# Kernel optimization log

Measured on AMD Instinct MI355X. Metric: run time of the kernel, lower is better.

Reference implementation:

```python
import jax, jax.numpy as jnp
import numpy as np

B, S, D = 4, 1024, 1024
H = 16
HD = D // H  # 64
NPOS = 64


def setup_inputs() -> dict:
    key = jax.random.key(0)
    ks = jax.random.split(key, 12)
    f = lambda k, shape, s=0.02: jax.random.normal(k, shape, dtype=jnp.float32) * s
    return {
        "q": jax.random.normal(ks[0], (B, S, D), dtype=jnp.float32),
        "k": jax.random.normal(ks[1], (B, S, D), dtype=jnp.float32),
        "v": jax.random.normal(ks[2], (B, S, D), dtype=jnp.float32),
        "Wq_w": f(ks[3], (D, D)), "Wq_b": f(ks[4], (D,)),
        "Wk_w": f(ks[5], (D, D)), "Wk_b": f(ks[6], (D,)),
        "Wv_w": f(ks[7], (D, D)), "Wv_b": f(ks[8], (D,)),
        "Wo_w": f(ks[9], (D, D)), "Wo_b": f(ks[10], (D,)),
        "pos_emb": f(ks[11], (HD, NPOS)),  # torch param is [1,1,head_dim,npos_max]
    }


def _proj(x, w, b):
    # nn.Linear: x @ w.T + b, then split heads -> [B, H, S, HD]
    y = jnp.einsum("bsd,ed->bse", x, w) + b
    bsz, s, _ = y.shape
    return y.reshape(bsz, s, H, HD).transpose(0, 2, 1, 3)


def reference(q, k, v, Wq_w, Wq_b, Wk_w, Wk_b, Wv_w, Wv_b, Wo_w, Wo_b, pos_emb):
    Q = _proj(q, Wq_w, Wq_b)
    K = _proj(k, Wk_w, Wk_b)
    V = _proj(v, Wv_w, Wv_b)

    scale = 1.0 / np.sqrt(HD).astype(np.float32)
    logits = jnp.einsum("bhqd,bhkd->bhqk", Q, K) * scale  # [B,H,S,S]

    # CoPE: sigmoid gates -> reverse cumsum -> interpolated position-logit gather
    gates = jax.nn.sigmoid(logits)
    pos = jnp.flip(jnp.cumsum(jnp.flip(gates, axis=-1), axis=-1), axis=-1)
    pos = jnp.minimum(pos, NPOS - 1)
    pos_floor = jnp.floor(pos)
    pos_ceil = jnp.ceil(pos)
    logits_int = jnp.einsum("bhqd,dn->bhqn", Q, pos_emb)  # [B,H,S,NPOS]
    lc = jnp.take_along_axis(logits_int, pos_ceil.astype(jnp.int32), axis=-1)
    lf = jnp.take_along_axis(logits_int, pos_floor.astype(jnp.int32), axis=-1)
    w = pos - pos_floor
    logits = logits + lc * w + lf * (1.0 - w)

    score = jax.nn.softmax(logits, axis=-1)
    out = jnp.einsum("bhqk,bhkd->bhqd", score, V)
    out = out.transpose(0, 2, 1, 3).reshape(q.shape[0], q.shape[1], D)
    return jnp.einsum("bsd,ed->bse", out, Wo_w) + Wo_b
```

## Files before the change

### kernel.cpp

```cpp
#include <hip/hip_runtime.h>
#include <hip/hip_bf16.h>

typedef __attribute__((ext_vector_type(8))) short short8;
typedef __attribute__((ext_vector_type(4))) float f32x4;
typedef unsigned short us;

#define MFMA16(a,b,c) __builtin_amdgcn_mfma_f32_16x16x32_bf16((a),(b),(c),0,0,0)
#define LOG2E 1.4426950408889634f

static __device__ __forceinline__ us bf16r(float x){
  unsigned u = __builtin_bit_cast(unsigned, x);
  u = u + 0x7fffu + ((u >> 16) & 1u);
  return (us)(u >> 16);
}
static __device__ __forceinline__ unsigned cvtpk(float a, float b){
  unsigned r; asm("v_cvt_pk_bf16_f32 %0, %1, %2" : "=v"(r) : "v"(a), "v"(b)); return r;
}
static __device__ __forceinline__ short8 cvt8(float4 a, float4 b){
  uint4 u; u.x = cvtpk(a.x, a.y); u.y = cvtpk(a.z, a.w);
  u.z = cvtpk(b.x, b.y); u.w = cvtpk(b.z, b.w);
  return __builtin_bit_cast(short8, u);
}
static __device__ __forceinline__ float b2f(us h){
  return __builtin_bit_cast(float, (unsigned)h << 16);
}
static __device__ __forceinline__ float exp2fast(float x){
  float r; asm("v_exp_f32 %0, %1" : "=v"(r) : "v"(x)); return r;
}
static __device__ __forceinline__ float rcpfast(float x){
  float r; asm("v_rcp_f32 %0, %1" : "=v"(r) : "v"(x)); return r;
}
static __device__ __forceinline__ float fractfast(float x){
  float r; asm("v_fract_f32 %0, %1" : "=v"(r) : "v"(x)); return r;
}

__global__ __launch_bounds__(256)
void transpose_pe(const float* __restrict__ pe, us* __restrict__ peT){
  const int t = threadIdx.x;
  const int n = t & 63, dq = t >> 6;
#pragma unroll
  for (int j = 0; j < 16; ++j){
    const int d = dq * 16 + j;
    peT[n * 64 + d] = bf16r(pe[d * 64 + n] * LOG2E);
  }
}

__global__ __launch_bounds__(256)
void transpose_v(const us* __restrict__ Vb, us* __restrict__ VT){
  __shared__ __align__(16) us tile[64 * 72];
  const int t = threadIdx.x;
  const int stile = blockIdx.x & 15;
  const int bh = blockIdx.x >> 4;
  const int b = bh >> 4, h = bh & 15;
  const int s0 = stile << 6;
#pragma unroll
  for (int c = 0; c < 2; ++c){
    const int idx = t + (c << 8);
    const int sr = idx >> 3, cw = idx & 7;
    *(short8*)&tile[sr * 72 + cw * 8] =
        *(const short8*)(Vb + ((size_t)(b * 1024 + s0 + sr)) * 1024 + h * 64 + cw * 8);
  }
  __syncthreads();
#pragma unroll
  for (int c = 0; c < 2; ++c){
    const int idx = t + (c << 8);
    const int dr = idx >> 3, sw = idx & 7;
    short8 o;
#pragma unroll
    for (int j = 0; j < 8; ++j) o[j] = (short)tile[(sw * 8 + j) * 72 + dr];
    *(short8*)(VT + ((size_t)(bh * 64 + dr)) * 1024 + s0 + sw * 8) = o;
  }
}

template<bool A_BF16, bool OUT_BF16>
__global__ __launch_bounds__(256)
void gemm3(const void* __restrict__ Av0, const void* __restrict__ Av1, const void* __restrict__ Av2,
           const float* __restrict__ W0, const float* __restrict__ W1, const float* __restrict__ W2,
           const float* __restrict__ bp0, const float* __restrict__ bp1, const float* __restrict__ bp2,
           void* __restrict__ O0, void* __restrict__ O1, void* __restrict__ O2){
  __shared__ __align__(16) us Al[128 * 64];
  __shared__ __align__(16) us Bl[128 * 64];
  const int sel = blockIdx.y;
  const void* Av   = sel == 0 ? Av0 : (sel == 1 ? Av1 : Av2);
  const float* Wm  = sel == 0 ? W0  : (sel == 1 ? W1  : W2);
  const float* bias = sel == 0 ? bp0 : (sel == 1 ? bp1 : bp2);
  void* Ov         = sel == 0 ? O0  : (sel == 1 ? O1  : O2);
  const int tid = threadIdx.x;
  const int bm = blockIdx.x & 31, bn = blockIdx.x >> 5;
  const int m0 = bm << 7, n0 = bn << 7;
  const int w = tid >> 6, l = tid & 63;
  const int lr = l & 15, lg = l >> 4;
  const int wm = (w & 1) << 6, wn = (w >> 1) << 6;
  int srow[4], scol[4], sdst[4];
#pragma unroll
  for (int c = 0; c < 4; ++c){
    const int idx = tid + (c << 8);
    const int r = idx >> 3, cw = idx & 7;
    srow[c] = r; scol[c] = cw << 3;
    sdst[c] = r * 64 + ((cw << 3) ^ ((r & 7) << 3));
  }
  const int swz = (lr & 7) << 3;
  f32x4 acc[4][4];
#pragma unroll
  for (int i = 0; i < 4; ++i)
#pragma unroll
    for (int j = 0; j < 4; ++j) acc[i][j] = (f32x4){0.f, 0.f, 0.f, 0.f};

  auto ldA = [&](int c, int k) -> short8 {
    if constexpr (A_BF16){
      return *(const short8*)((const us*)Av + (size_t)(m0 + srow[c]) * 1024 + k + scol[c]);
    } else {
      const float* p = (const float*)Av + (size_t)(m0 + srow[c]) * 1024 + k + scol[c];
      return cvt8(*(const float4*)p, *(const float4*)(p + 4));
    }
  };
  auto ldW = [&](int c, int k) -> short8 {
    const float* p = Wm + (size_t)(n0 + srow[c]) * 1024 + k + scol[c];
    return cvt8(*(const float4*)p, *(const float4*)(p + 4));
  };

  short8 av[4], bv[4];
#pragma unroll
  for (int c = 0; c < 4; ++c){ av[c] = ldA(c, 0); bv[c] = ldW(c, 0); }

  for (int k0 = 0; k0 < 1024; k0 += 64){
    __syncthreads();
#pragma unroll
    for (int c = 0; c < 4; ++c){
      *(short8*)&Al[sdst[c]] = av[c];
      *(short8*)&Bl[sdst[c]] = bv[c];
    }
    __syncthreads();
    if (k0 < 960){
#pragma unroll
      for (int c = 0; c < 4; ++c){ av[c] = ldA(c, k0 + 64); bv[c] = ldW(c, k0 + 64); }
    }
#pragma unroll
    for (int ks = 0; ks < 2; ++ks){
      short8 af[4], bfv[4];
#pragma unroll
      for (int mt = 0; mt < 4; ++mt)
        af[mt] = *(const short8*)&Al[(wm + mt * 16 + lr) * 64 + (((ks << 5) + (lg << 3)) ^ swz)];
#pragma unroll
      for (int nt = 0; nt < 4; ++nt)
        bfv[nt] = *(const short8*)&Bl[(wn + nt * 16 + lr) * 64 + (((ks << 5) + (lg << 3)) ^ swz)];
#pragma unroll
      for (int mt = 0; mt < 4; ++mt)
#pragma unroll
        for (int nt = 0; nt < 4; ++nt)
          acc[mt][nt] = MFMA16(af[mt], bfv[nt], acc[mt][nt]);
    }
  }
  float bb[4];
#pragma unroll
  for (int nt = 0; nt < 4; ++nt) bb[nt] = bias[n0 + wn + nt * 16 + lr];
#pragma unroll
  for (int mt = 0; mt < 4; ++mt)
#pragma unroll
    for (int nt = 0; nt < 4; ++nt)
#pragma unroll
      for (int r = 0; r < 4; ++r){
        const size_t m = m0 + wm + mt * 16 + lg * 4 + r;
        const size_t n = n0 + wn + nt * 16 + lr;
        const float vv = acc[mt][nt][r] + bb[nt];
        if (OUT_BF16) ((us*)Ov)[m * 1024 + n] = bf16r(vv);
        else          ((float*)Ov)[m * 1024 + n] = vv;
      }
}

__global__ __launch_bounds__(256, 5)
void cope_attn_v6(const us* __restrict__ Qb, const us* __restrict__ Kb,
                  const us* __restrict__ VT, const us* __restrict__ peT,
                  us* __restrict__ Ob){
  __shared__ __align__(16) us yl[16 * 1024];
  const int tid = threadIdx.x;
  const int w = tid >> 6, l = tid & 63;
  const int lr = l & 15, lg = l >> 4;
  const int qt = blockIdx.x & 63;
  const int bh = blockIdx.x >> 6;
  const int b = bh >> 4, h = bh & 15;
  const int q0 = qt << 4;
  const us* Qh = Qb + ((size_t)(b * 1024 + q0)) * 1024 + h * 64;
  const us* Kh = Kb + ((size_t)(b * 1024)) * 1024 + h * 64;
  const us* Vh = VT + ((size_t)bh) * 64 * 1024;
  const float QSC = 0.125f * LOG2E;

  const short8 aq0 = *(const short8*)(Qh + (size_t)lr * 1024 + lg * 8);
  const short8 aq1 = *(const short8*)(Qh + (size_t)lr * 1024 + 32 + lg * 8);

  {
    f32x4 a = (f32x4){0.f, 0.f, 0.f, 0.f};
    const short8 p0 = *(const short8*)(peT + (size_t)(w * 16 + lr) * 64 + lg * 8);
    const short8 p1 = *(const short8*)(peT + (size_t)(w * 16 + lr) * 64 + 32 + lg * 8);
    a = MFMA16(aq0, p0, a);
    a = MFMA16(aq1, p1, a);
#pragma unroll
    for (int r = 0; r < 4; ++r) yl[(lg * 4 + r) * 64 + w * 16 + lr] = bf16r(a[r]);
  }
  __syncthreads();
  unsigned trow[4];
#pragma unroll
  for (int rr = 0; rr < 4; ++rr){
    const int row = w * 4 + rr;
    const us lov = yl[row * 64 + l];
    const us hiv = (l < 63) ? yl[row * 64 + l + 1] : lov;
    const float dif = b2f(hiv) - b2f(lov);
    trow[rr] = (unsigned)lov | ((unsigned)bf16r(dif) << 16);
  }
  __syncthreads();
  {
    const int kbase = w << 8;
    const us* Kw = Kh + (size_t)(kbase + lr) * 1024 + lg * 8;
    short8 b0 = *(const short8*)(Kw);
    short8 b1 = *(const short8*)(Kw + 32);
    for (int t = 0; t < 16; ++t){
      short8 n0v = b0, n1v = b1;
      if (t < 15){
        const us* Kn = Kw + (size_t)((t + 1) * 16) * 1024;
        n0v = *(const short8*)(Kn);
        n1v = *(const short8*)(Kn + 32);
      }
      f32x4 a = (f32x4){0.f, 0.f, 0.f, 0.f};
      a = MFMA16(aq0, b0, a);
      a = MFMA16(aq1, b1, a);
      const int kc = kbase + t * 16 + lr;
      const unsigned p01 = cvtpk(a[0] * QSC, a[1] * QSC);
      const unsigned p23 = cvtpk(a[2] * QSC, a[3] * QSC);
      const int r0 = lg * 4;
      yl[(r0 + 0) * 1024 + (((kc >> 3) ^ ((r0 + 0) & 7)) << 3) + (kc & 7)] = (us)p01;
      yl[(r0 + 1) * 1024 + (((kc >> 3) ^ ((r0 + 1) & 7)) << 3) + (kc & 7)] = (us)(p01 >> 16);
      yl[(r0 + 2) * 1024 + (((kc >> 3) ^ ((r0 + 2) & 7)) << 3) + (kc & 7)] = (us)p23;
      yl[(r0 + 3) * 1024 + (((kc >> 3) ^ ((r0 + 3) & 7)) << 3) + (kc & 7)] = (us)(p23 >> 16);
      b0 = n0v; b1 = n1v;
    }
  }
  __syncthreads();
#pragma unroll
  for (int rr = 0; rr < 4; ++rr){
    const int row = w * 4 + rr;
    const int sz = row & 7;
    const int ad0 = row * 1024 + (((2 * l) ^ sz) << 3);
    const int ad1 = row * 1024 + (((2 * l + 1) ^ sz) << 3);
    const short8 y0 = *(const short8*)&yl[ad0];
    const short8 y1 = *(const short8*)&yl[ad1];
    float x[16];
#pragma unroll
    for (int j = 0; j < 8; ++j){ x[j] = b2f((us)y0[j]); x[8 + j] = b2f((us)y1[j]); }
    float pref[16];
    float s = 0.f;
#pragma unroll
    for (int i = 0; i < 16; ++i){
      const float g = rcpfast(1.f + exp2fast(-x[i]));
      pref[i] = s;
      s += g;
    }
    float run = s;
#pragma unroll
    for (int off = 1; off < 64; off <<= 1){
      const float t2 = __shfl_up(run, off);
      if (l >= off) run += t2;
    }
    const float T = __shfl(run, 63);
    const float base = T - (run - s);
    const unsigned tbl = trow[rr];
    float sum = 0.f;
#pragma unroll
    for (int i = 0; i < 16; ++i){
      float p = base - pref[i];
      p = __builtin_amdgcn_fmed3f(p, 0.f, 63.f);
      const int il = (int)p;
      const float wt = fractfast(p);
      const unsigned pr = (unsigned)__builtin_amdgcn_ds_bpermute(il << 2, (int)tbl);
      const float lo  = __builtin_bit_cast(float, pr << 16);
      const float dif = __builtin_bit_cast(float, pr & 0xffff0000u);
      const float e = exp2fast(x[i] + lo + wt * dif);
      x[i] = e;
      sum += e;
    }
#pragma unroll
    for (int off = 1; off < 64; off <<= 1) sum += __shfl_xor(sum, off);
    const float inv = rcpfast(sum);
    uint4 ua, ub;
    ua.x = cvtpk(x[0] * inv,  x[1] * inv);  ua.y = cvtpk(x[2] * inv,  x[3] * inv);
    ua.z = cvtpk(x[4] * inv,  x[5] * inv);  ua.w = cvtpk(x[6] * inv,  x[7] * inv);
    ub.x = cvtpk(x[8] * inv,  x[9] * inv);  ub.y = cvtpk(x[10] * inv, x[11] * inv);
    ub.z = cvtpk(x[12] * inv, x[13] * inv); ub.w = cvtpk(x[14] * inv, x[15] * inv);
    *(uint4*)&yl[ad0] = ua;
    *(uint4*)&yl[ad1] = ub;
  }
  __syncthreads();
  {
    const int d0 = w * 16;
    const int psw = lr & 7;
    f32x4 a = (f32x4){0.f, 0.f, 0.f, 0.f};
    const us* Vw = Vh + (size_t)(d0 + lr) * 1024 + lg * 8;
    short8 vb = *(const short8*)(Vw);
    for (int ks = 0; ks < 32; ++ks){
      short8 vn = vb;
      if (ks < 31) vn = *(const short8*)(Vw + (ks + 1) * 32);
      const short8 pa = *(const short8*)&yl[lr * 1024 + ((((ks << 2) + lg) ^ psw) << 3)];
      a = MFMA16(pa, vb, a);
      vb = vn;
    }
#pragma unroll
    for (int r = 0; r < 4; ++r)
      Ob[((size_t)(b * 1024 + q0 + lg * 4 + r)) * 1024 + h * 64 + d0 + lr] = bf16r(a[r]);
  }
}

extern "C" void kernel_launch(void* const* d_in, const int* in_sizes, int n_in,
                              void* d_out, int out_size, void* d_ws, size_t ws_size,
                              hipStream_t stream) {
  const float* q    = (const float*)d_in[0];
  const float* k    = (const float*)d_in[1];
  const float* v    = (const float*)d_in[2];
  const float* Wq_w = (const float*)d_in[3];
  const float* Wq_b = (const float*)d_in[4];
  const float* Wk_w = (const float*)d_in[5];
  const float* Wk_b = (const float*)d_in[6];
  const float* Wv_w = (const float*)d_in[7];
  const float* Wv_b = (const float*)d_in[8];
  const float* Wo_w = (const float*)d_in[9];
  const float* Wo_b = (const float*)d_in[10];
  const float* pe   = (const float*)d_in[11];
  float* out = (float*)d_out;

  char* W = (char*)d_ws;
  const size_t MB = (size_t)1 << 20;
  us* Qbf = (us*)(W);
  us* Kbf = (us*)(W + 8 * MB);
  us* Vbf = (us*)(W + 16 * MB);
  us* VTb = (us*)(W + 24 * MB);
  us* Obf = (us*)(W + 32 * MB);
  us* peT = (us*)(W + 40 * MB);

  transpose_pe<<<1, 256, 0, stream>>>(pe, peT);
  gemm3<false, true><<<dim3(256, 3), 256, 0, stream>>>(
      q, k, v, Wq_w, Wk_w, Wv_w, Wq_b, Wk_b, Wv_b, Qbf, Kbf, Vbf);
  transpose_v<<<1024, 256, 0, stream>>>(Vbf, VTb);
  cope_attn_v6<<<4096, 256, 0, stream>>>(Qbf, Kbf, VTb, peT, Obf);
  gemm3<true, false><<<dim3(256, 1), 256, 0, stream>>>(
      Obf, Obf, Obf, Wo_w, Wo_w, Wo_w, Wo_b, Wo_b, Wo_b, out, out, out);
}
```

Baseline: 221.1 us.

## Split attention key range into two chunks to halve LDS and raise occupancy

The attention kernel now processes the 1024 keys in two 512-key chunks, last chunk first. A carry of the reverse cumulative gate sum links the chunks, and the unnormalized softmax numerators are accumulated into the PV output. Normalization is deferred to the end using per-row sums kept in shared memory. This halves the LDS score buffer (32KB to 16KB) and raises launch bounds from 5 to 7 blocks per CU to improve occupancy. The costs are extra barriers and an unnormalized exp without max subtraction, so overflow risk is unchanged but bf16 rounding now happens before normalization.

```diff
diff --git a/kernel.cpp b/kernel.cpp
--- a/kernel.cpp
+++ b/kernel.cpp
@@ -168,11 +168,12 @@
       }
 }
 
-__global__ __launch_bounds__(256, 5)
-void cope_attn_v6(const us* __restrict__ Qb, const us* __restrict__ Kb,
+__global__ __launch_bounds__(256, 7)
+void cope_attn_v7(const us* __restrict__ Qb, const us* __restrict__ Kb,
                   const us* __restrict__ VT, const us* __restrict__ peT,
                   us* __restrict__ Ob){
-  __shared__ __align__(16) us yl[16 * 1024];
+  __shared__ __align__(16) us yl[16 * 512];
+  __shared__ float sums[16];
   const int tid = threadIdx.x;
   const int w = tid >> 6, l = tid & 63;
   const int lr = l & 15, lg = l >> 4;
@@ -207,104 +208,113 @@
     const float dif = b2f(hiv) - b2f(lov);
     trow[rr] = (unsigned)lov | ((unsigned)bf16r(dif) << 16);
   }
+
+  float carry[4] = {0.f, 0.f, 0.f, 0.f};
+  float rsum[4]  = {0.f, 0.f, 0.f, 0.f};
+  f32x4 oacc = (f32x4){0.f, 0.f, 0.f, 0.f};
+  const int d0 = w * 16;
+  const int psw = lr & 7;
+
+  for (int c = 1; c >= 0; --c){
+    const int koff = c << 9;
+    __syncthreads();
+    {
+      const int kbase = w << 7;
+      const us* Kw = Kh + (size_t)(koff + kbase + lr) * 1024 + lg * 8;
+      short8 b0 = *(const short8*)(Kw);
+      short8 b1 = *(const short8*)(Kw + 32);
+      for (int t = 0; t < 8; ++t){
+        short8 n0v = b0, n1v = b1;
+        if (t < 7){
+          const us* Kn = Kw + (size_t)((t + 1) * 16) * 1024;
+          n0v = *(const short8*)(Kn);
+          n1v = *(const short8*)(Kn + 32);
+        }
+        f32x4 a = (f32x4){0.f, 0.f, 0.f, 0.f};
+        a = MFMA16(aq0, b0, a);
+        a = MFMA16(aq1, b1, a);
+        const int kc = kbase + t * 16 + lr;
+        const unsigned p01 = cvtpk(a[0] * QSC, a[1] * QSC);
+        const unsigned p23 = cvtpk(a[2] * QSC, a[3] * QSC);
+        const int r0 = lg * 4;
+        yl[(r0 + 0) * 512 + (((kc >> 3) ^ ((r0 + 0) & 7)) << 3) + (kc & 7)] = (us)p01;
+        yl[(r0 + 1) * 512 + (((kc >> 3) ^ ((r0 + 1) & 7)) << 3) + (kc & 7)] = (us)(p01 >> 16);
+        yl[(r0 + 2) * 512 + (((kc >> 3) ^ ((r0 + 2) & 7)) << 3) + (kc & 7)] = (us)p23;
+        yl[(r0 + 3) * 512 + (((kc >> 3) ^ ((r0 + 3) & 7)) << 3) + (kc & 7)] = (us)(p23 >> 16);
+        b0 = n0v; b1 = n1v;
+      }
+    }
+    __syncthreads();
+#pragma unroll
+    for (int rr = 0; rr < 4; ++rr){
+      const int row = w * 4 + rr;
+      const int ad = row * 512 + ((l ^ (row & 7)) << 3);
+      const short8 y0 = *(const short8*)&yl[ad];
+      float x[8];
+#pragma unroll
+      for (int j = 0; j < 8; ++j) x[j] = b2f((us)y0[j]);
+      float pref[8];
+      float s = 0.f;
+#pragma unroll
+      for (int i = 0; i < 8; ++i){
+        const float g = rcpfast(1.f + exp2fast(-x[i]));
+        pref[i] = s;
+        s += g;
+      }
+      float run = s;
+#pragma unroll
+      for (int off = 1; off < 64; off <<= 1){
+        const float t2 = __shfl_up(run, off);
+        if (l >= off) run += t2;
+      }
+      const float T = __shfl(run, 63);
+      const float base = carry[rr] + T - (run - s);
+      carry[rr] += T;
+      const unsigned tbl = trow[rr];
+      float sum = 0.f;
+#pragma unroll
+      for (int i = 0; i < 8; ++i){
+        float p = base - pref[i];
+        p = __builtin_amdgcn_fmed3f(p, 0.f, 63.f);
+        const int il = (int)p;
+        const float wt = fractfast(p);
+        const unsigned pr = (unsigned)__builtin_amdgcn_ds_bpermute(il << 2, (int)tbl);
+        const float lo  = __builtin_bit_cast(float, pr << 16);
+        const float dif = __builtin_bit_cast(float, pr & 0xffff0000u);
+        const float e = exp2fast(x[i] + lo + wt * dif);
+        x[i] = e;
+        sum += e;
+      }
+      rsum[rr] += sum;
+      uint4 ua;
+      ua.x = cvtpk(x[0], x[1]); ua.y = cvtpk(x[2], x[3]);
+      ua.z = cvtpk(x[4], x[5]); ua.w = cvtpk(x[6], x[7]);
+      *(uint4*)&yl[ad] = ua;
+      if (c == 0){
+        float rs = rsum[rr];
+#pragma unroll
+        for (int off = 1; off < 64; off <<= 1) rs += __shfl_xor(rs, off);
+        if (l == 0) sums[row] = rs;
+      }
+    }
+    __syncthreads();
+    {
+      const us* Vw = Vh + (size_t)(d0 + lr) * 1024 + koff + lg * 8;
+      short8 vb = *(const short8*)(Vw);
+      for (int ks = 0; ks < 16; ++ks){
+        short8 vn = vb;
+        if (ks < 15) vn = *(const short8*)(Vw + (ks + 1) * 32);
+        const short8 pa = *(const short8*)&yl[lr * 512 + ((((ks << 2) + lg) ^ psw) << 3)];
+        oacc = MFMA16(pa, vb, oacc);
+        vb = vn;
+      }
+    }
+  }
   __syncthreads();
-  {
-    const int kbase = w << 8;
-    const us* Kw = Kh + (size_t)(kbase + lr) * 1024 + lg * 8;
-    short8 b0 = *(const short8*)(Kw);
-    short8 b1 = *(const short8*)(Kw + 32);
-    for (int t = 0; t < 16; ++t){
-      short8 n0v = b0, n1v = b1;
-      if (t < 15){
-        const us* Kn = Kw + (size_t)((t + 1) * 16) * 1024;
-        n0v = *(const short8*)(Kn);
-        n1v = *(const short8*)(Kn + 32);
-      }
-      f32x4 a = (f32x4){0.f, 0.f, 0.f, 0.f};
-      a = MFMA16(aq0, b0, a);
-      a = MFMA16(aq1, b1, a);
-      const int kc = kbase + t * 16 + lr;
-      const unsigned p01 = cvtpk(a[0] * QSC, a[1] * QSC);
-      const unsigned p23 = cvtpk(a[2] * QSC, a[3] * QSC);
-      const int r0 = lg * 4;
-      yl[(r0 + 0) * 1024 + (((kc >> 3) ^ ((r0 + 0) & 7)) << 3) + (kc & 7)] = (us)p01;
-      yl[(r0 + 1) * 1024 + (((kc >> 3) ^ ((r0 + 1) & 7)) << 3) + (kc & 7)] = (us)(p01 >> 16);
-      yl[(r0 + 2) * 1024 + (((kc >> 3) ^ ((r0 + 2) & 7)) << 3) + (kc & 7)] = (us)p23;
-      yl[(r0 + 3) * 1024 + (((kc >> 3) ^ ((r0 + 3) & 7)) << 3) + (kc & 7)] = (us)(p23 >> 16);
-      b0 = n0v; b1 = n1v;
-    }
-  }
-  __syncthreads();
-#pragma unroll
-  for (int rr = 0; rr < 4; ++rr){
-    const int row = w * 4 + rr;
-    const int sz = row & 7;
-    const int ad0 = row * 1024 + (((2 * l) ^ sz) << 3);
-    const int ad1 = row * 1024 + (((2 * l + 1) ^ sz) << 3);
-    const short8 y0 = *(const short8*)&yl[ad0];
-    const short8 y1 = *(const short8*)&yl[ad1];
-    float x[16];
-#pragma unroll
-    for (int j = 0; j < 8; ++j){ x[j] = b2f((us)y0[j]); x[8 + j] = b2f((us)y1[j]); }
-    float pref[16];
-    float s = 0.f;
-#pragma unroll
-    for (int i = 0; i < 16; ++i){
-      const float g = rcpfast(1.f + exp2fast(-x[i]));
-      pref[i] = s;
-      s += g;
-    }
-    float run = s;
-#pragma unroll
-    for (int off = 1; off < 64; off <<= 1){
-      const float t2 = __shfl_up(run, off);
-      if (l >= off) run += t2;
-    }
-    const float T = __shfl(run, 63);
-    const float base = T - (run - s);
-    const unsigned tbl = trow[rr];
-    float sum = 0.f;
-#pragma unroll
-    for (int i = 0; i < 16; ++i){
-      float p = base - pref[i];
-      p = __builtin_amdgcn_fmed3f(p, 0.f, 63.f);
-      const int il = (int)p;
-      const float wt = fractfast(p);
-      const unsigned pr = (unsigned)__builtin_amdgcn_ds_bpermute(il << 2, (int)tbl);
-      const float lo  = __builtin_bit_cast(float, pr << 16);
-      const float dif = __builtin_bit_cast(float, pr & 0xffff0000u);
-      const float e = exp2fast(x[i] + lo + wt * dif);
-      x[i] = e;
-      sum += e;
-    }
-#pragma unroll
-    for (int off = 1; off < 64; off <<= 1) sum += __shfl_xor(sum, off);
-    const float inv = rcpfast(sum);
-    uint4 ua, ub;
-    ua.x = cvtpk(x[0] * inv,  x[1] * inv);  ua.y = cvtpk(x[2] * inv,  x[3] * inv);
-    ua.z = cvtpk(x[4] * inv,  x[5] * inv);  ua.w = cvtpk(x[6] * inv,  x[7] * inv);
-    ub.x = cvtpk(x[8] * inv,  x[9] * inv);  ub.y = cvtpk(x[10] * inv, x[11] * inv);
-    ub.z = cvtpk(x[12] * inv, x[13] * inv); ub.w = cvtpk(x[14] * inv, x[15] * inv);
-    *(uint4*)&yl[ad0] = ua;
-    *(uint4*)&yl[ad1] = ub;
-  }
-  __syncthreads();
-  {
-    const int d0 = w * 16;
-    const int psw = lr & 7;
-    f32x4 a = (f32x4){0.f, 0.f, 0.f, 0.f};
-    const us* Vw = Vh + (size_t)(d0 + lr) * 1024 + lg * 8;
-    short8 vb = *(const short8*)(Vw);
-    for (int ks = 0; ks < 32; ++ks){
-      short8 vn = vb;
-      if (ks < 31) vn = *(const short8*)(Vw + (ks + 1) * 32);
-      const short8 pa = *(const short8*)&yl[lr * 1024 + ((((ks << 2) + lg) ^ psw) << 3)];
-      a = MFMA16(pa, vb, a);
-      vb = vn;
-    }
-#pragma unroll
-    for (int r = 0; r < 4; ++r)
-      Ob[((size_t)(b * 1024 + q0 + lg * 4 + r)) * 1024 + h * 64 + d0 + lr] = bf16r(a[r]);
+#pragma unroll
+  for (int r = 0; r < 4; ++r){
+    const float inv = rcpfast(sums[lg * 4 + r]);
+    Ob[((size_t)(b * 1024 + q0 + lg * 4 + r)) * 1024 + h * 64 + d0 + lr] = bf16r(oacc[r] * inv);
   }
 }
 
@@ -338,7 +348,7 @@
   gemm3<false, true><<<dim3(256, 3), 256, 0, stream>>>(
       q, k, v, Wq_w, Wk_w, Wv_w, Wq_b, Wk_b, Wv_b, Qbf, Kbf, Vbf);
   transpose_v<<<1024, 256, 0, stream>>>(Vbf, VTb);
-  cope_attn_v6<<<4096, 256, 0, stream>>>(Qbf, Kbf, VTb, peT, Obf);
+  cope_attn_v7<<<4096, 256, 0, stream>>>(Qbf, Kbf, VTb, peT, Obf);
   gemm3<true, false><<<dim3(256, 1), 256, 0, stream>>>(
       Obf, Obf, Obf, Wo_w, Wo_w, Wo_w, Wo_b, Wo_b, Wo_b, out, out, out);
 }
```

Result: slower. 287.8 us (+30.2%).
